# Optimization experiments

Hardware: AMD Instinct MI355X
Metric: run time of the kernel (lower is better)

The kernel has to match this reference:

```python
import jax, jax.numpy as jnp
import numpy as np

N_NODES = 100000
N_EDGES = 1600000
D = 128


def _deg_inv_sqrt(idx, num_nodes):
    deg = jax.ops.segment_sum(jnp.ones_like(idx, dtype=jnp.float32), idx, num_segments=num_nodes)
    deg = jnp.clip(deg, 1.0, None)  # DGL clamps degree to min 1
    return deg ** -0.5


def graph_conv(x, W, b, src, dst, out_norm, in_norm, relu):
    # norm='both': scale by src out-degree^{-1/2}, transform, aggregate, scale by dst in-degree^{-1/2}
    h = x * out_norm[:, None]
    h = h @ W                               # [N, d_out]
    m = jax.ops.segment_sum(h[src], dst, num_segments=x.shape[0])  # sparse A^T h
    m = m * in_norm[:, None] + b
    return jax.nn.relu(m) if relu else m


def setup_inputs() -> dict:
    key = jax.random.key(0)
    ks = jax.random.split(key, 8)
    s = 1.0 / np.sqrt(D)
    return {
        "node_feats": jax.random.normal(ks[0], (N_NODES, D), dtype=jnp.float32),
        "src": jax.random.randint(ks[1], (N_EDGES,), 0, N_NODES, dtype=jnp.int32),
        "dst": jax.random.randint(ks[2], (N_EDGES,), 0, N_NODES, dtype=jnp.int32),
        "W1": jax.random.normal(ks[3], (D, D), dtype=jnp.float32) * s,
        "b1": jnp.zeros((D,), jnp.float32),
        "W2": jax.random.normal(ks[4], (D, D), dtype=jnp.float32) * s,
        "b2": jnp.zeros((D,), jnp.float32),
        "res_W": jax.random.normal(ks[5], (D, D), dtype=jnp.float32) * s,
        "mlp_W": jax.random.normal(ks[6], (D, 2), dtype=jnp.float32) * s,
        "mlp_b": jnp.zeros((2,), jnp.float32),
    }


def reference(node_feats, src, dst, W1, b1, W2, b2, res_W, mlp_W, mlp_b):
    out_norm = _deg_inv_sqrt(src, node_feats.shape[0])  # out-degree of source nodes
    in_norm = _deg_inv_sqrt(dst, node_feats.shape[0])   # in-degree of dest nodes
    h = graph_conv(node_feats, W1, b1, src, dst, out_norm, in_norm, relu=True)
    # dropout p=0.0 -> identity
    h = graph_conv(h, W2, b2, src, dst, out_norm, in_norm, relu=False)
    # residual (res_fc is Linear without bias)
    h = h + node_feats @ res_W
    # final MLP head -> logits [N, 2]
    return h @ mlp_W + mlp_b
```

## Files before the change

### kernel.cpp

```cpp
#include <hip/hip_runtime.h>
#include <stdint.h>

__device__ __forceinline__ float bflo(unsigned int u) {
    union { unsigned int u; float f; } c; c.u = u << 16; return c.f;
}
__device__ __forceinline__ float bfhi(unsigned int u) {
    union { unsigned int u; float f; } c; c.u = u & 0xffff0000u; return c.f;
}
__device__ __forceinline__ unsigned int f2bf(float f) {
    union { float f; unsigned int u; } c; c.f = f;
    unsigned int u = c.u;
    u += 0x7fffu + ((u >> 16) & 1u);
    return u >> 16;
}
__device__ __forceinline__ unsigned int packbf(float a, float b) {
    return f2bf(a) | (f2bf(b) << 16);
}

typedef __attribute__((ext_vector_type(8))) short s8v;
typedef __attribute__((ext_vector_type(4))) float f4v;
typedef __attribute__((ext_vector_type(2))) float f2v;

__device__ __forceinline__ f4v mfma16(s8v a, s8v b, f4v c) {
    return __builtin_amdgcn_mfma_f32_16x16x32_bf16(a, b, c, 0, 0, 0);
}

__device__ __forceinline__ unsigned char f2fp8(float v) {
    return (unsigned char)(__builtin_amdgcn_cvt_pk_fp8_f32(v, v, 0, false) & 0xff);
}

#define RANGE_BITS 15
#define RANGE (1 << RANGE_BITS)
#define NR 4
#define NSLICE 64

__global__ __launch_bounds__(256) void k_prep_w(const float* __restrict__ W1,
                                                const float* __restrict__ W2,
                                                const float* __restrict__ Wr,
                                                unsigned short* __restrict__ Wt) {
    const float* W = (blockIdx.x == 0) ? W1 : (blockIdx.x == 1) ? W2 : Wr;
    unsigned short* T = Wt + (size_t)blockIdx.x * 16384;
    const int wv = threadIdx.x >> 6, l = threadIdx.x & 63;
    const int kb = blockIdx.y * 32 + wv * 8;
#pragma unroll
    for (int half = 0; half < 2; ++half) {
        const int n = l + half * 64;
        unsigned short tmp[8];
#pragma unroll
        for (int j = 0; j < 8; ++j) tmp[j] = (unsigned short)f2bf(W[(size_t)(kb + j) * 128 + n]);
#pragma unroll
        for (int j = 0; j < 8; j += 2)
            *(unsigned int*)&T[(size_t)n * 128 + kb + j] =
                (unsigned int)tmp[j] | ((unsigned int)tmp[j + 1] << 16);
    }
}

__global__ __launch_bounds__(64) void k_prep_k(const float* __restrict__ b2,
                                               const float* __restrict__ mlpW,
                                               const float* __restrict__ mlpB,
                                               float* __restrict__ K) {
    const int l = threadIdx.x;
    float p0 = b2[l] * mlpW[l * 2 + 0] + b2[l + 64] * mlpW[(l + 64) * 2 + 0];
    float p1 = b2[l] * mlpW[l * 2 + 1] + b2[l + 64] * mlpW[(l + 64) * 2 + 1];
#pragma unroll
    for (int off = 32; off > 0; off >>= 1) {
        p0 += __shfl_xor(p0, off);
        p1 += __shfl_xor(p1, off);
    }
    if (l == 0) { K[0] = p0 + mlpB[0]; K[1] = p1 + mlpB[1]; }
}

__global__ __launch_bounds__(256) void k_hist_lds(const int* __restrict__ src,
                                                  const int* __restrict__ dst,
                                                  unsigned int* __restrict__ partialS,
                                                  unsigned int* __restrict__ partialD,
                                                  int E, int EPS) {
    __shared__ unsigned int cnt[RANGE / 2];
    const int r = blockIdx.x & (NR - 1);
    const int s = blockIdx.x >> 2;
    const int a = blockIdx.y;
    const int* __restrict__ arr = a ? dst : src;
    unsigned int* part = (a ? partialD : partialS)
                         + ((size_t)r * NSLICE + s) * (RANGE / 2);
    for (int i = threadIdx.x; i < RANGE / 2; i += 256) cnt[i] = 0;
    __syncthreads();
    const int e0 = s * EPS;
    const int e1 = min(E, e0 + EPS);
    int e = e0 + threadIdx.x * 4;
    for (; e + 3 < e1; e += 1024) {
        const int4 v = *(const int4*)&arr[e];
        if ((v.x >> RANGE_BITS) == r) { int l = v.x & (RANGE - 1); atomicAdd(&cnt[l >> 1], 1u << ((l & 1) << 4)); }
        if ((v.y >> RANGE_BITS) == r) { int l = v.y & (RANGE - 1); atomicAdd(&cnt[l >> 1], 1u << ((l & 1) << 4)); }
        if ((v.z >> RANGE_BITS) == r) { int l = v.z & (RANGE - 1); atomicAdd(&cnt[l >> 1], 1u << ((l & 1) << 4)); }
        if ((v.w >> RANGE_BITS) == r) { int l = v.w & (RANGE - 1); atomicAdd(&cnt[l >> 1], 1u << ((l & 1) << 4)); }
    }
    for (; e < e1; ++e) {
        const int idx = arr[e];
        if ((idx >> RANGE_BITS) == r) { int l = idx & (RANGE - 1); atomicAdd(&cnt[l >> 1], 1u << ((l & 1) << 4)); }
    }
    __syncthreads();
    for (int i = threadIdx.x; i < RANGE / 2; i += 256) part[i] = cnt[i];
}

__global__ __launch_bounds__(256) void k_deg_reduce(unsigned int* __restrict__ pS,
                                                    unsigned int* __restrict__ pD,
                                                    float* __restrict__ out_norm,
                                                    float* __restrict__ in_norm,
                                                    int* __restrict__ in_deg, int N) {
    const int a = blockIdx.y;
    const int t = blockIdx.x * 256 + threadIdx.x;
    const int r = t >> (RANGE_BITS - 1);
    const int w = t & ((RANGE / 2) - 1);
    unsigned int* base = (a ? pD : pS) + (size_t)r * NSLICE * (RANGE / 2) + w;
    unsigned int lo = 0, hi = 0;
    if (a) {
        for (int s = 0; s < NSLICE; ++s) {
            const unsigned int v = base[(size_t)s * (RANGE / 2)];
            base[(size_t)s * (RANGE / 2)] = lo | (hi << 16);
            lo += v & 0xffffu; hi += v >> 16;
        }
    } else {
        for (int s = 0; s < NSLICE; ++s) {
            const unsigned int v = base[(size_t)s * (RANGE / 2)];
            lo += v & 0xffffu; hi += v >> 16;
        }
    }
    const int n0 = r * RANGE + 2 * w, n1 = n0 + 1;
    if (a) {
        if (n0 < N) { in_deg[n0] = (int)lo; in_norm[n0] = rsqrtf(fmaxf((float)lo, 1.f)); }
        if (n1 < N) { in_deg[n1] = (int)hi; in_norm[n1] = rsqrtf(fmaxf((float)hi, 1.f)); }
    } else {
        if (n0 < N) out_norm[n0] = rsqrtf(fmaxf((float)lo, 1.f));
        if (n1 < N) out_norm[n1] = rsqrtf(fmaxf((float)hi, 1.f));
    }
}

__global__ __launch_bounds__(1024) void k_scan_block(const int* __restrict__ in,
                                                     int* __restrict__ row_ptr,
                                                     int* __restrict__ partials, int n) {
    __shared__ int sh[1024];
    int i = blockIdx.x * 1024 + threadIdx.x;
    int v = (i < n) ? in[i] : 0;
    sh[threadIdx.x] = v;
    __syncthreads();
    for (int off = 1; off < 1024; off <<= 1) {
        int t = (threadIdx.x >= off) ? sh[threadIdx.x - off] : 0;
        __syncthreads();
        sh[threadIdx.x] += t;
        __syncthreads();
    }
    if (i < n) row_ptr[i + 1] = sh[threadIdx.x];
    if (threadIdx.x == 1023) partials[blockIdx.x] = sh[1023];
}

__global__ __launch_bounds__(1024) void k_scan_partials(int* __restrict__ partials, int nb) {
    __shared__ int sh[1024];
    int v = (threadIdx.x < nb) ? partials[threadIdx.x] : 0;
    sh[threadIdx.x] = v;
    __syncthreads();
    for (int off = 1; off < 1024; off <<= 1) {
        int t = (threadIdx.x >= off) ? sh[threadIdx.x - off] : 0;
        __syncthreads();
        sh[threadIdx.x] += t;
        __syncthreads();
    }
    if (threadIdx.x < nb) partials[threadIdx.x] = sh[threadIdx.x] - v;
}

__global__ void k_scan_finalize(int* __restrict__ row_ptr, const int* __restrict__ partials,
                                int n) {
    int i = blockIdx.x * blockDim.x + threadIdx.x;
    if (i < n) {
        row_ptr[i + 1] += partials[i >> 10];
        if (i == 0) row_ptr[0] = 0;
    }
}

__global__ __launch_bounds__(256) void k_scatter_lds(const int* __restrict__ src,
                                                     const int* __restrict__ dst,
                                                     const unsigned int* __restrict__ pD,
                                                     const int* __restrict__ row_ptr,
                                                     int* __restrict__ ssrc, int E, int EPS) {
    __shared__ unsigned int cur[RANGE / 2];
    const int r = blockIdx.x & (NR - 1);
    const int s = blockIdx.x >> 2;
    const unsigned int* pre = pD + ((size_t)r * NSLICE + s) * (RANGE / 2);
    for (int i = threadIdx.x; i < RANGE / 2; i += 256) cur[i] = pre[i];
    __syncthreads();
    const int e0 = s * EPS;
    const int e1 = min(E, e0 + EPS);
    int e = e0 + threadIdx.x * 4;
    for (; e + 3 < e1; e += 1024) {
        const int4 v = *(const int4*)&dst[e];
#pragma unroll
        for (int j = 0; j < 4; ++j) {
            const int d = (&v.x)[j];
            if ((d >> RANGE_BITS) == r) {
                const int local = d & (RANGE - 1);
                const int sh = (local & 1) << 4;
                const unsigned int old = atomicAdd(&cur[local >> 1], 1u << sh);
                const unsigned int off = (old >> sh) & 0xffffu;
                ssrc[row_ptr[d] + (int)off] = src[e + j];
            }
        }
    }
    for (; e < e1; ++e) {
        const int d = dst[e];
        if ((d >> RANGE_BITS) == r) {
            const int local = d & (RANGE - 1);
            const int sh = (local & 1) << 4;
            const unsigned int old = atomicAdd(&cur[local >> 1], 1u << sh);
            const unsigned int off = (old >> sh) & 0xffffu;
            ssrc[row_ptr[d] + (int)off] = src[e];
        }
    }
}

template <typename TIN, int MODE>
__global__ __launch_bounds__(256) void gemm_mfma(const TIN* __restrict__ X,
                                                 const unsigned short* __restrict__ Wt0,
                                                 const unsigned short* __restrict__ Wt1,
                                                 const float* __restrict__ scale,
                                                 unsigned char* __restrict__ out_table,
                                                 float2* __restrict__ outv,
                                                 const float* __restrict__ mlpW,
                                                 int N) {
    constexpr int NW = (MODE == 0) ? 2 : 1;
    __shared__ unsigned short Ws[NW][128 * 128];
    const int tid = threadIdx.x;
#pragma unroll
    for (int w = 0; w < NW; ++w) {
        const unsigned short* Wsrc = w ? Wt1 : Wt0;
        for (int i = tid; i < 2048; i += 256) {
            const int n = i >> 4, b = i & 15;
            const uint4 v = *(const uint4*)&Wsrc[(size_t)n * 128 + b * 8];
            *(uint4*)&Ws[w][n * 128 + ((b ^ (n & 15)) << 3)] = v;
        }
    }
    __syncthreads();

    const int lane = tid & 63;
    const int wave = tid >> 6;
    const int quad = lane >> 4;
    const int l16 = lane & 15;
    const int r_base = blockIdx.x * 64 + wave * 16;
    const int ra = min(r_base + l16, N - 1);

    f4v acc[NW][8];
#pragma unroll
    for (int w = 0; w < NW; ++w)
#pragma unroll
        for (int nn = 0; nn < 8; ++nn) acc[w][nn] = (f4v)0.f;

    const TIN* xp = X + (size_t)ra * 128 + quad * 8;

#pragma unroll
    for (int kt = 0; kt < 4; ++kt) {
        s8v af;
        if constexpr (sizeof(TIN) == 4) {
            const float4 lo = *(const float4*)(xp + kt * 32);
            const float4 hi = *(const float4*)(xp + kt * 32 + 4);
            af[0] = (short)f2bf(lo.x); af[1] = (short)f2bf(lo.y);
            af[2] = (short)f2bf(lo.z); af[3] = (short)f2bf(lo.w);
            af[4] = (short)f2bf(hi.x); af[5] = (short)f2bf(hi.y);
            af[6] = (short)f2bf(hi.z); af[7] = (short)f2bf(hi.w);
        } else {
            af = *(const s8v*)(xp + kt * 32);
        }
#pragma unroll
        for (int nn = 0; nn < 8; ++nn) {
            const int bofs = (nn * 16 + l16) * 128 + (((kt * 4 + quad) ^ l16) << 3);
#pragma unroll
            for (int w = 0; w < NW; ++w) {
                const s8v bf = *(const s8v*)&Ws[w][bofs];
                acc[w][nn] = mfma16(af, bf, acc[w][nn]);
            }
        }
    }

    const int rc = r_base + quad * 4;
    float sc[4];
#pragma unroll
    for (int g = 0; g < 4; ++g) sc[g] = scale[min(rc + g, N - 1)];

    if constexpr (MODE == 0) {
#pragma unroll
        for (int nn = 0; nn < 8; ++nn) {
            const int col = nn * 16 + l16;
#pragma unroll
            for (int g = 0; g < 4; ++g) {
                const int r = rc + g;
                if (r < N) out_table[(size_t)r * 128 + col] = f2fp8(acc[0][nn][g] * sc[g]);
            }
        }
    }

    {
        float2 w2[8];
#pragma unroll
        for (int nn = 0; nn < 8; ++nn)
            w2[nn] = ((const float2*)mlpW)[nn * 16 + l16];
#pragma unroll
        for (int g = 0; g < 4; ++g) {
            float p0 = 0.f, p1 = 0.f;
#pragma unroll
            for (int nn = 0; nn < 8; ++nn) {
                float val;
                if constexpr (MODE == 0) val = acc[1][nn][g];
                else                     val = acc[0][nn][g] * sc[g];
                p0 = fmaf(val, w2[nn].x, p0);
                p1 = fmaf(val, w2[nn].y, p1);
            }
#pragma unroll
            for (int off = 1; off < 16; off <<= 1) {
                p0 += __shfl_xor(p0, off);
                p1 += __shfl_xor(p1, off);
            }
            const int r = rc + g;
            if (l16 == 0 && r < N) outv[r] = make_float2(p0, p1);
        }
    }
}

__global__ __launch_bounds__(256) void k_spmm1(const unsigned char* __restrict__ T,
                                               const int* __restrict__ row_ptr,
                                               const int* __restrict__ ssrc,
                                               const float* __restrict__ in_norm,
                                               const float* __restrict__ bias,
                                               unsigned short* __restrict__ Hout, int N) {
    const int lane = threadIdx.x & 63;
    const int grp = lane >> 4;
    const int gl  = lane & 15;
    const int d = blockIdx.x * 4 + (threadIdx.x >> 6);
    if (d >= N) return;

    const int start = row_ptr[d], end = row_ptr[d + 1];
    float acc[8];
#pragma unroll
    for (int j = 0; j < 8; ++j) acc[j] = 0.f;

    for (int base = start; base < end; base += 64) {
        const int cnt = min(64, end - base);
        const int sl = (lane < cnt) ? ssrc[base + lane] : 0;
        for (int i = 0; i < cnt; i += 16) {
            int   ss[4];
            float mm[4];
            uint2 ww[4];
#pragma unroll
            for (int u = 0; u < 4; ++u) {
                const int e = i + 4 * u + grp;
                ss[u] = __shfl(sl, min(e, cnt - 1));
                mm[u] = (e < cnt) ? 1.f : 0.f;
            }
#pragma unroll
            for (int u = 0; u < 4; ++u)
                ww[u] = *(const uint2*)&T[(size_t)ss[u] * 128 + gl * 8];
#pragma unroll
            for (int u = 0; u < 4; ++u) {
                const f2v a0 = __builtin_amdgcn_cvt_pk_f32_fp8(ww[u].x, false);
                const f2v a1 = __builtin_amdgcn_cvt_pk_f32_fp8(ww[u].x, true);
                const f2v a2 = __builtin_amdgcn_cvt_pk_f32_fp8(ww[u].y, false);
                const f2v a3 = __builtin_amdgcn_cvt_pk_f32_fp8(ww[u].y, true);
                const float m = mm[u];
                acc[0] = fmaf(m, a0[0], acc[0]); acc[1] = fmaf(m, a0[1], acc[1]);
                acc[2] = fmaf(m, a1[0], acc[2]); acc[3] = fmaf(m, a1[1], acc[3]);
                acc[4] = fmaf(m, a2[0], acc[4]); acc[5] = fmaf(m, a2[1], acc[5]);
                acc[6] = fmaf(m, a3[0], acc[6]); acc[7] = fmaf(m, a3[1], acc[7]);
            }
        }
    }

#pragma unroll
    for (int j = 0; j < 8; ++j) {
        acc[j] += __shfl_xor(acc[j], 16);
        acc[j] += __shfl_xor(acc[j], 32);
    }

    const float inr = in_norm[d];
    const float4 bb0 = *(const float4*)&bias[gl * 8];
    const float4 bb1 = *(const float4*)&bias[gl * 8 + 4];
    float v[8];
    v[0] = fmaxf(acc[0] * inr + bb0.x, 0.f); v[1] = fmaxf(acc[1] * inr + bb0.y, 0.f);
    v[2] = fmaxf(acc[2] * inr + bb0.z, 0.f); v[3] = fmaxf(acc[3] * inr + bb0.w, 0.f);
    v[4] = fmaxf(acc[4] * inr + bb1.x, 0.f); v[5] = fmaxf(acc[5] * inr + bb1.y, 0.f);
    v[6] = fmaxf(acc[6] * inr + bb1.z, 0.f); v[7] = fmaxf(acc[7] * inr + bb1.w, 0.f);

    if (grp == 0) {
        uint4 o;
        o.x = packbf(v[0], v[1]); o.y = packbf(v[2], v[3]);
        o.z = packbf(v[4], v[5]); o.w = packbf(v[6], v[7]);
        *(uint4*)&Hout[(size_t)d * 128 + gl * 8] = o;
    }
}

__global__ __launch_bounds__(256) void k_final(const float2* __restrict__ u,
                                               const int* __restrict__ row_ptr,
                                               const int* __restrict__ ssrc,
                                               const float* __restrict__ in_norm,
                                               const float2* __restrict__ v,
                                               const float* __restrict__ K,
                                               float2* __restrict__ out, int N) {
    const int d = blockIdx.x * 256 + threadIdx.x;
    if (d >= N) return;
    const int start = row_ptr[d], end = row_ptr[d + 1];
    float sx = 0.f, sy = 0.f;
    int i = start;
    for (; i + 4 <= end; i += 4) {
        const int s0 = ssrc[i], s1 = ssrc[i + 1], s2 = ssrc[i + 2], s3 = ssrc[i + 3];
        const float2 u0 = u[s0], u1 = u[s1], u2 = u[s2], u3 = u[s3];
        sx += (u0.x + u1.x) + (u2.x + u3.x);
        sy += (u0.y + u1.y) + (u2.y + u3.y);
    }
    for (; i < end; ++i) {
        const float2 uu = u[ssrc[i]];
        sx += uu.x; sy += uu.y;
    }
    const float inr = in_norm[d];
    const float2 vv = v[d];
    out[d] = make_float2(sx * inr + vv.x + K[0], sy * inr + vv.y + K[1]);
}

extern "C" void kernel_launch(void* const* d_in, const int* in_sizes, int n_in,
                              void* d_out, int out_size, void* d_ws, size_t ws_size,
                              hipStream_t stream) {
    const float* x     = (const float*)d_in[0];
    const int*   src   = (const int*)d_in[1];
    const int*   dst   = (const int*)d_in[2];
    const float* W1    = (const float*)d_in[3];
    const float* b1    = (const float*)d_in[4];
    const float* W2    = (const float*)d_in[5];
    const float* b2    = (const float*)d_in[6];
    const float* res_W = (const float*)d_in[7];
    const float* mlp_W = (const float*)d_in[8];
    const float* mlp_b = (const float*)d_in[9];
    float* out = (float*)d_out;

    const int N = in_sizes[0] / 128;
    const int E = in_sizes[1];
    const int EPS = (E + NSLICE - 1) / NSLICE;

    char* p = (char*)d_ws;
    unsigned char*  A = (unsigned char*)p;   p += (size_t)N * 128;
    unsigned short* B = (unsigned short*)p;  p += (size_t)N * 128 * 2;
    unsigned short* Wt = (unsigned short*)p; p += (size_t)3 * 16384 * 2;
    float* out_norm = (float*)p;             p += (size_t)N * 4;
    float* in_norm  = (float*)p;             p += (size_t)N * 4;
    int* in_deg     = (int*)p;               p += (size_t)N * 4;
    int* row_ptr    = (int*)p;               p += (size_t)(N + 1) * 4;
    int* scanpart   = (int*)p;               p += (size_t)1024 * 4;
    float* Kc       = (float*)p;             p += (size_t)16;
    float2* v2      = (float2*)p;            p += (size_t)N * 8;
    float2* u2      = (float2*)p;            p += (size_t)N * 8;
    int* ssrc       = (int*)p;               p += (size_t)E * 4;
    unsigned int* partialS = (unsigned int*)A;
    unsigned int* partialD = (unsigned int*)((char*)B + (size_t)4 * 1024 * 1024);

    const int gN = (N + 255) / 256;
    const int nb = (N + 1023) / 1024;
    const int gGemm = (N + 63) / 64;
    const int gSpmm = (N + 3) / 4;

    k_prep_w<<<dim3(3, 4), 256, 0, stream>>>(W1, W2, res_W, Wt);
    k_prep_k<<<1, 64, 0, stream>>>(b2, mlp_W, mlp_b, Kc);

    k_hist_lds<<<dim3(NR * NSLICE, 2), 256, 0, stream>>>(src, dst, partialS, partialD, E, EPS);
    k_deg_reduce<<<dim3(NR * (RANGE / 2) / 256, 2), 256, 0, stream>>>(partialS, partialD,
                                                                      out_norm, in_norm, in_deg, N);

    k_scan_block<<<nb, 1024, 0, stream>>>(in_deg, row_ptr, scanpart, N);
    k_scan_partials<<<1, 1024, 0, stream>>>(scanpart, nb);
    k_scan_finalize<<<gN, 256, 0, stream>>>(row_ptr, scanpart, N);
    k_scatter_lds<<<NR * NSLICE, 256, 0, stream>>>(src, dst, partialD, row_ptr, ssrc, E, EPS);

    gemm_mfma<float, 0><<<gGemm, 256, 0, stream>>>(x, Wt, Wt + 2 * 16384, out_norm,
                                                   A, v2, mlp_W, N);

    k_spmm1<<<gSpmm, 256, 0, stream>>>(A, row_ptr, ssrc, in_norm, b1, B, N);

    gemm_mfma<unsigned short, 1><<<gGemm, 256, 0, stream>>>(B, Wt + 16384, nullptr, out_norm,
                                                            nullptr, u2, mlp_W, N);

    k_final<<<gN, 256, 0, stream>>>(u2, row_ptr, ssrc, in_norm, v2, Kc, (float2*)out, N);

    (void)n_in; (void)out_size; (void)ws_size;
}
```

Baseline: 280.0 us.

## Fold W2 and res_W into mlp_W to replace second GEMM with GEMV

Precomputes G = res_W@mlp_W and W2@mlp_W (128x2 each). The residual projection becomes a small fp32 dot product inside the first GEMM, and the second MFMA GEMM becomes a light GEMV kernel over the bf16 hidden state. This removes one full 128x128 weight set from LDS and the MFMA work of the second layer. It is algebraically exact up to the order of rounding; the residual path now uses fp32 inputs instead of bf16.

```diff
diff --git a/kernel.cpp b/kernel.cpp
--- a/kernel.cpp
+++ b/kernel.cpp
@@ -3,9 +3,6 @@
 
 __device__ __forceinline__ float bflo(unsigned int u) {
     union { unsigned int u; float f; } c; c.u = u << 16; return c.f;
-}
-__device__ __forceinline__ float bfhi(unsigned int u) {
-    union { unsigned int u; float f; } c; c.u = u & 0xffff0000u; return c.f;
 }
 __device__ __forceinline__ unsigned int f2bf(float f) {
     union { float f; unsigned int u; } c; c.f = f;
@@ -35,11 +32,9 @@
 #define NSLICE 64
 
 __global__ __launch_bounds__(256) void k_prep_w(const float* __restrict__ W1,
-                                                const float* __restrict__ W2,
-                                                const float* __restrict__ Wr,
                                                 unsigned short* __restrict__ Wt) {
-    const float* W = (blockIdx.x == 0) ? W1 : (blockIdx.x == 1) ? W2 : Wr;
-    unsigned short* T = Wt + (size_t)blockIdx.x * 16384;
+    const float* W = W1;
+    unsigned short* T = Wt;
     const int wv = threadIdx.x >> 6, l = threadIdx.x & 63;
     const int kb = blockIdx.y * 32 + wv * 8;
 #pragma unroll
@@ -53,6 +48,23 @@
             *(unsigned int*)&T[(size_t)n * 128 + kb + j] =
                 (unsigned int)tmp[j] | ((unsigned int)tmp[j + 1] << 16);
     }
+}
+
+__global__ __launch_bounds__(128) void k_prep_g(const float* __restrict__ Wr,
+                                                const float* __restrict__ W2,
+                                                const float* __restrict__ mlpW,
+                                                float* __restrict__ G) {
+    const float* W = blockIdx.x ? W2 : Wr;
+    float* o = G + blockIdx.x * 256;
+    const int k = threadIdx.x;
+    float g0 = 0.f, g1 = 0.f;
+    for (int j = 0; j < 128; ++j) {
+        const float w = W[k * 128 + j];
+        g0 = fmaf(w, mlpW[j * 2 + 0], g0);
+        g1 = fmaf(w, mlpW[j * 2 + 1], g1);
+    }
+    o[k * 2 + 0] = g0;
+    o[k * 2 + 1] = g1;
 }
 
 __global__ __launch_bounds__(64) void k_prep_k(const float* __restrict__ b2,
@@ -216,27 +228,22 @@
     }
 }
 
-template <typename TIN, int MODE>
-__global__ __launch_bounds__(256) void gemm_mfma(const TIN* __restrict__ X,
-                                                 const unsigned short* __restrict__ Wt0,
-                                                 const unsigned short* __restrict__ Wt1,
-                                                 const float* __restrict__ scale,
-                                                 unsigned char* __restrict__ out_table,
-                                                 float2* __restrict__ outv,
-                                                 const float* __restrict__ mlpW,
-                                                 int N) {
-    constexpr int NW = (MODE == 0) ? 2 : 1;
-    __shared__ unsigned short Ws[NW][128 * 128];
+__global__ __launch_bounds__(256) void k_gemm1(const float* __restrict__ X,
+                                               const unsigned short* __restrict__ Wt0,
+                                               const float* __restrict__ scale,
+                                               const float* __restrict__ G,
+                                               unsigned char* __restrict__ out_table,
+                                               float2* __restrict__ outv,
+                                               int N) {
+    __shared__ unsigned short Ws[128 * 128];
+    __shared__ float2 gr[128];
     const int tid = threadIdx.x;
-#pragma unroll
-    for (int w = 0; w < NW; ++w) {
-        const unsigned short* Wsrc = w ? Wt1 : Wt0;
-        for (int i = tid; i < 2048; i += 256) {
-            const int n = i >> 4, b = i & 15;
-            const uint4 v = *(const uint4*)&Wsrc[(size_t)n * 128 + b * 8];
-            *(uint4*)&Ws[w][n * 128 + ((b ^ (n & 15)) << 3)] = v;
-        }
-    }
+    for (int i = tid; i < 2048; i += 256) {
+        const int n = i >> 4, b = i & 15;
+        const uint4 v = *(const uint4*)&Wt0[(size_t)n * 128 + b * 8];
+        *(uint4*)&Ws[n * 128 + ((b ^ (n & 15)) << 3)] = v;
+    }
+    if (tid < 128) gr[tid] = ((const float2*)G)[tid];
     __syncthreads();
 
     const int lane = tid & 63;
@@ -246,78 +253,55 @@
     const int r_base = blockIdx.x * 64 + wave * 16;
     const int ra = min(r_base + l16, N - 1);
 
-    f4v acc[NW][8];
-#pragma unroll
-    for (int w = 0; w < NW; ++w)
-#pragma unroll
-        for (int nn = 0; nn < 8; ++nn) acc[w][nn] = (f4v)0.f;
-
-    const TIN* xp = X + (size_t)ra * 128 + quad * 8;
+    f4v acc[8];
+#pragma unroll
+    for (int nn = 0; nn < 8; ++nn) acc[nn] = (f4v)0.f;
+    float p0 = 0.f, p1 = 0.f;
+
+    const float* xp = X + (size_t)ra * 128 + quad * 8;
 
 #pragma unroll
     for (int kt = 0; kt < 4; ++kt) {
+        const float4 lo = *(const float4*)(xp + kt * 32);
+        const float4 hi = *(const float4*)(xp + kt * 32 + 4);
+        {
+            const int kb = kt * 32 + quad * 8;
+            const float xv[8] = {lo.x, lo.y, lo.z, lo.w, hi.x, hi.y, hi.z, hi.w};
+#pragma unroll
+            for (int j = 0; j < 8; ++j) {
+                const float2 g = gr[kb + j];
+                p0 = fmaf(xv[j], g.x, p0);
+                p1 = fmaf(xv[j], g.y, p1);
+            }
+        }
         s8v af;
-        if constexpr (sizeof(TIN) == 4) {
-            const float4 lo = *(const float4*)(xp + kt * 32);
-            const float4 hi = *(const float4*)(xp + kt * 32 + 4);
-            af[0] = (short)f2bf(lo.x); af[1] = (short)f2bf(lo.y);
-            af[2] = (short)f2bf(lo.z); af[3] = (short)f2bf(lo.w);
-            af[4] = (short)f2bf(hi.x); af[5] = (short)f2bf(hi.y);
-            af[6] = (short)f2bf(hi.z); af[7] = (short)f2bf(hi.w);
-        } else {
-            af = *(const s8v*)(xp + kt * 32);
-        }
+        af[0] = (short)f2bf(lo.x); af[1] = (short)f2bf(lo.y);
+        af[2] = (short)f2bf(lo.z); af[3] = (short)f2bf(lo.w);
+        af[4] = (short)f2bf(hi.x); af[5] = (short)f2bf(hi.y);
+        af[6] = (short)f2bf(hi.z); af[7] = (short)f2bf(hi.w);
 #pragma unroll
         for (int nn = 0; nn < 8; ++nn) {
             const int bofs = (nn * 16 + l16) * 128 + (((kt * 4 + quad) ^ l16) << 3);
-#pragma unroll
-            for (int w = 0; w < NW; ++w) {
-                const s8v bf = *(const s8v*)&Ws[w][bofs];
-                acc[w][nn] = mfma16(af, bf, acc[w][nn]);
-            }
-        }
-    }
+            const s8v bf = *(const s8v*)&Ws[bofs];
+            acc[nn] = mfma16(af, bf, acc[nn]);
+        }
+    }
+
+    p0 += __shfl_xor(p0, 16); p0 += __shfl_xor(p0, 32);
+    p1 += __shfl_xor(p1, 16); p1 += __shfl_xor(p1, 32);
+    if (quad == 0 && r_base + l16 < N) outv[r_base + l16] = make_float2(p0, p1);
 
     const int rc = r_base + quad * 4;
     float sc[4];
 #pragma unroll
     for (int g = 0; g < 4; ++g) sc[g] = scale[min(rc + g, N - 1)];
-
-    if constexpr (MODE == 0) {
-#pragma unroll
-        for (int nn = 0; nn < 8; ++nn) {
-            const int col = nn * 16 + l16;
-#pragma unroll
-            for (int g = 0; g < 4; ++g) {
-                const int r = rc + g;
-                if (r < N) out_table[(size_t)r * 128 + col] = f2fp8(acc[0][nn][g] * sc[g]);
-            }
-        }
-    }
-
-    {
-        float2 w2[8];
-#pragma unroll
-        for (int nn = 0; nn < 8; ++nn)
-            w2[nn] = ((const float2*)mlpW)[nn * 16 + l16];
+#pragma unroll
+    for (int nn = 0; nn < 8; ++nn) {
+        const int col = nn * 16 + l16;
 #pragma unroll
         for (int g = 0; g < 4; ++g) {
-            float p0 = 0.f, p1 = 0.f;
-#pragma unroll
-            for (int nn = 0; nn < 8; ++nn) {
-                float val;
-                if constexpr (MODE == 0) val = acc[1][nn][g];
-                else                     val = acc[0][nn][g] * sc[g];
-                p0 = fmaf(val, w2[nn].x, p0);
-                p1 = fmaf(val, w2[nn].y, p1);
-            }
-#pragma unroll
-            for (int off = 1; off < 16; off <<= 1) {
-                p0 += __shfl_xor(p0, off);
-                p1 += __shfl_xor(p1, off);
-            }
             const int r = rc + g;
-            if (l16 == 0 && r < N) outv[r] = make_float2(p0, p1);
+            if (r < N) out_table[(size_t)r * 128 + col] = f2fp8(acc[nn][g] * sc[g]);
         }
     }
 }
@@ -390,6 +374,38 @@
         o.x = packbf(v[0], v[1]); o.y = packbf(v[2], v[3]);
         o.z = packbf(v[4], v[5]); o.w = packbf(v[6], v[7]);
         *(uint4*)&Hout[(size_t)d * 128 + gl * 8] = o;
+    }
+}
+
+__global__ __launch_bounds__(256) void k_gemv2(const unsigned short* __restrict__ B,
+                                               const float* __restrict__ onorm,
+                                               const float* __restrict__ G,
+                                               float2* __restrict__ u2, int N) {
+    const int tid = threadIdx.x;
+    const int lane = tid & 63;
+    const int gl = lane & 15;
+    const int rg = lane >> 4;
+    const int row = blockIdx.x * 16 + (tid >> 6) * 4 + rg;
+    const float2* G2 = (const float2*)(G + 256);
+    float p0 = 0.f, p1 = 0.f;
+    if (row < N) {
+        const s8v bv = *(const s8v*)&B[(size_t)row * 128 + gl * 8];
+#pragma unroll
+        for (int j = 0; j < 8; ++j) {
+            const float xv = bflo((unsigned int)(unsigned short)bv[j]);
+            const float2 g = G2[gl * 8 + j];
+            p0 = fmaf(xv, g.x, p0);
+            p1 = fmaf(xv, g.y, p1);
+        }
+    }
+#pragma unroll
+    for (int off = 1; off < 16; off <<= 1) {
+        p0 += __shfl_xor(p0, off);
+        p1 += __shfl_xor(p1, off);
+    }
+    if (gl == 0 && row < N) {
+        const float s = onorm[row];
+        u2[row] = make_float2(p0 * s, p1 * s);
     }
 }
 
@@ -454,13 +470,16 @@
     int* ssrc       = (int*)p;               p += (size_t)E * 4;
     unsigned int* partialS = (unsigned int*)A;
     unsigned int* partialD = (unsigned int*)((char*)B + (size_t)4 * 1024 * 1024);
+    float* G = (float*)(scanpart + 512);
 
     const int gN = (N + 255) / 256;
     const int nb = (N + 1023) / 1024;
     const int gGemm = (N + 63) / 64;
     const int gSpmm = (N + 3) / 4;
-
-    k_prep_w<<<dim3(3, 4), 256, 0, stream>>>(W1, W2, res_W, Wt);
+    const int gGemv = (N + 15) / 16;
+
+    k_prep_w<<<dim3(1, 4), 256, 0, stream>>>(W1, Wt);
+    k_prep_g<<<2, 128, 0, stream>>>(res_W, W2, mlp_W, G);
     k_prep_k<<<1, 64, 0, stream>>>(b2, mlp_W, mlp_b, Kc);
 
     k_hist_lds<<<dim3(NR * NSLICE, 2), 256, 0, stream>>>(src, dst, partialS, partialD, E, EPS);
@@ -472,13 +491,11 @@
     k_scan_finalize<<<gN, 256, 0, stream>>>(row_ptr, scanpart, N);
     k_scatter_lds<<<NR * NSLICE, 256, 0, stream>>>(src, dst, partialD, row_ptr, ssrc, E, EPS);
 
-    gemm_mfma<float, 0><<<gGemm, 256, 0, stream>>>(x, Wt, Wt + 2 * 16384, out_norm,
-                                                   A, v2, mlp_W, N);
+    k_gemm1<<<gGemm, 256, 0, stream>>>(x, Wt, out_norm, G, A, v2, N);
 
     k_spmm1<<<gSpmm, 256, 0, stream>>>(A, row_ptr, ssrc, in_norm, b1, B, N);
 
-    gemm_mfma<unsigned short, 1><<<gGemm, 256, 0, stream>>>(B, Wt + 16384, nullptr, out_norm,
-                                                            nullptr, u2, mlp_W, N);
+    k_gemv2<<<gGemv, 256, 0, stream>>>(B, out_norm, G, u2, N);
 
     k_final<<<gN, 256, 0, stream>>>(u2, row_ptr, ssrc, in_norm, v2, Kc, (float2*)out, N);
 
```

Measured after the change: 265.9 us. 1.05x faster.
